# Optimization experiments

Hardware: AMD Instinct MI355X
Metric: run time of the kernel (lower is better)

Reference implementation:

```python
import jax, jax.numpy as jnp
import numpy as np
from jax import lax

T, B, H, L = 512, 64, 512, 2  # seq_len, batch, hidden(=input), num_layers


def setup_inputs() -> dict:
    key = jax.random.key(0)
    ks = jax.random.split(key, 6)
    s = 1.0 / np.sqrt(H)  # torch default init scale
    x = jax.random.normal(ks[0], (T, B, H), dtype=jnp.float32)
    h0 = jax.random.normal(ks[1], (L, B, H), dtype=jnp.float32)
    W_ih = jax.random.uniform(ks[2], (L, H, H), jnp.float32, -s, s)
    W_hh = jax.random.uniform(ks[3], (L, H, H), jnp.float32, -s, s)
    b_ih = jax.random.uniform(ks[4], (L, H), jnp.float32, -s, s)
    b_hh = jax.random.uniform(ks[5], (L, H), jnp.float32, -s, s)
    return {"x": x, "h0": h0, "W_ih": W_ih, "W_hh": W_hh, "b_ih": b_ih, "b_hh": b_hh}


def _run_layer(x, h0, Wi, Wh, bi, bh):
    # Precompute input contribution for all timesteps: [T,B,H]
    xw = jnp.einsum('tbi,hi->tbh', x, Wi) + bi

    def step(h, xw_t):
        h_new = jnp.tanh(xw_t + h @ Wh.T + bh)
        return h_new, h_new

    h_last, ys = lax.scan(step, h0, xw)
    return ys, h_last


def reference(x, h0, W_ih, W_hh, b_ih, b_hh):
    # Multi-layer Elman RNN with tanh, matching torch.nn.RNN (batch_first=False).
    h_n = []
    out = x
    for l in range(L):
        out, h_last = _run_layer(out, h0[l], W_ih[l], W_hh[l], b_ih[l], b_hh[l])
        h_n.append(h_last)
    return out, jnp.stack(h_n, axis=0)
```

## Files before the change

### kernel.cpp

```cpp
#include <hip/hip_runtime.h>
#include <stdint.h>

#define T_ 512
#define B_ 64
#define H_ 512
#define L_ 2
#define TBH (T_*B_*H_)
#define BH  (B_*H_)
#define NC  8
#define CS  64
#define CROWS (CS*B_)
#define CSZ ((size_t)CROWS*H_)
#define WPK_OFF  ((size_t)4*CSZ)
#define WPK_U4L  (64*512)
#define WIHP_OFF (WPK_OFF + (size_t)2*WPK_U4L*4)
#define Y1_OFF   (WIHP_OFF + (size_t)262144)
#define Y1SZ     ((size_t)CROWS*H_)

typedef float    f32x4 __attribute__((ext_vector_type(4)));
typedef short    s16x8 __attribute__((ext_vector_type(8)));
typedef short    s16x4 __attribute__((ext_vector_type(4)));
typedef _Float16 h2    __attribute__((ext_vector_type(2)));

static __device__ __forceinline__ short f2bf(float f) {
  uint32_t u = __float_as_uint(f);
  u = (u + 0x7fffu + ((u >> 16) & 1u)) >> 16;
  return (short)u;
}

static __device__ __forceinline__ float fdot2(h2 a, h2 b, float c) {
#if __has_builtin(__builtin_amdgcn_fdot2)
  return __builtin_amdgcn_fdot2(a, b, c, false);
#else
  return c + (float)a[0] * (float)b[0] + (float)a[1] * (float)b[1];
#endif
}

template <int IMM>
static __device__ __forceinline__ float swz(float v) {
  return __int_as_float(__builtin_amdgcn_ds_swizzle(__float_as_int(v), IMM));
}

static __device__ __forceinline__ float dpp_xor1(float v) {
  return __int_as_float(__builtin_amdgcn_mov_dpp(__float_as_int(v), 0xB1, 0xF, 0xF, true));
}
static __device__ __forceinline__ float dpp_xor2(float v) {
  return __int_as_float(__builtin_amdgcn_mov_dpp(__float_as_int(v), 0x4E, 0xF, 0xF, true));
}

static __device__ __forceinline__ void rawbar() {
  __builtin_amdgcn_sched_barrier(0);
  asm volatile("s_waitcnt lgkmcnt(0)" ::: "memory");
  __builtin_amdgcn_s_barrier();
  __builtin_amdgcn_sched_barrier(0);
}

static __device__ __forceinline__ uint32_t pack2(float a, float b) {
  h2 p = { (_Float16)a, (_Float16)b };
  return __builtin_bit_cast(uint32_t, p);
}

static __device__ __forceinline__ h2 bch(uint32_t u) {
  return __builtin_bit_cast(h2, u);
}

__global__ __launch_bounds__(512, 1)
void prepack(const float* __restrict__ Whh, const float* __restrict__ Wih,
             const float* __restrict__ x, float* __restrict__ ws,
             float* __restrict__ out) {
  const int bid = blockIdx.x, tid = threadIdx.x;
  if (bid < 2) {
    const int l = bid, c = tid & 7, rg = tid >> 3;
    uint4* dst = (uint4*)(ws + WPK_OFF) + (size_t)l * WPK_U4L;
    const float* W = Whh + (size_t)l * H_ * H_;
    #pragma unroll
    for (int k = 0; k < 8; ++k) {
      const float* wrow = W + (size_t)(rg * 8 + k) * H_ + c * 64;
      #pragma unroll
      for (int u = 0; u < 6; ++u) {
        f32x4 w4 = *(const f32x4*)(wrow + u * 8);
        f32x4 w5 = *(const f32x4*)(wrow + u * 8 + 4);
        uint4 pk;
        pk.x = pack2(w4.x, w4.y);
        pk.y = pack2(w4.z, w4.w);
        pk.z = pack2(w5.x, w5.y);
        pk.w = pack2(w5.z, w5.w);
        dst[(k * 6 + u) * 512 + tid] = pk;
      }
      #pragma unroll
      for (int p = 0; p < 2; ++p) {
        f32x4 w4 = *(const f32x4*)(wrow + 48 + p * 8);
        f32x4 w5 = *(const f32x4*)(wrow + 48 + p * 8 + 4);
        uint4 pk;
        pk.x = pack2(w4.x, w4.y);
        pk.y = pack2(w4.z, w4.w);
        pk.z = pack2(w5.x, w5.y);
        pk.w = pack2(w5.z, w5.w);
        dst[(48 + k * 2 + p) * 512 + tid] = pk;
      }
    }
  } else if (bid < 4) {
    const int l = bid - 2;
    const float* src = Wih + (size_t)l * H_ * H_;
    short* dst = (short*)(ws + WIHP_OFF) + (size_t)l * H_ * H_;
    for (int it = 0; it < 64; ++it) {
      int e = (it * 512 + tid) * 8;
      f32x4 a = *(const f32x4*)(src + e);
      f32x4 b = *(const f32x4*)(src + e + 4);
      s16x8 p = { f2bf(a.x), f2bf(a.y), f2bf(a.z), f2bf(a.w),
                  f2bf(b.x), f2bf(b.y), f2bf(b.z), f2bf(b.w) };
      *(s16x8*)(dst + e) = p;
    }
  } else {
    const int w = bid - 4;
    const int cc = w >> 3, sub = w & 7;
    const float* src = x + (size_t)cc * CSZ + (size_t)sub * (CSZ / 8);
    short* dst = (short*)(out + (size_t)cc * CSZ) + (size_t)sub * (CSZ / 8);
    for (int it = 0; it < 64; ++it) {
      int e = (it * 512 + tid) * 8;
      f32x4 a = *(const f32x4*)(src + e);
      f32x4 b = *(const f32x4*)(src + e + 4);
      s16x8 p = { f2bf(a.x), f2bf(a.y), f2bf(a.z), f2bf(a.w),
                  f2bf(b.x), f2bf(b.y), f2bf(b.z), f2bf(b.w) };
      *(s16x8*)(dst + e) = p;
    }
  }
}

__device__ void gemm_role(char* smem, int rb,
                          const short* __restrict__ In,
                          const short* __restrict__ W,
                          const float* __restrict__ bi,
                          const float* __restrict__ bh,
                          float* __restrict__ Out) {
  constexpr int LDT = 40;
  short* As = (short*)smem;
  short* Bs = (short*)(smem + 256 * LDT * 2);

  const int tid  = threadIdx.x;
  const int m0   = (rb >> 2) * 256;
  const int n0   = (rb & 3) * 128;
  const int wave = tid >> 6, lane = tid & 63;
  const int wm   = (wave >> 1) * 64;
  const int wn   = (wave & 1) * 64;
  const int quad = lane >> 4, tq = lane & 15;

  f32x4 acc[4][4] = {};

  for (int k0 = 0; k0 < 512; k0 += 32) {
    #pragma unroll
    for (int v = 0; v < 2; ++v) {
      int idx = v * 512 + tid;
      int r = idx >> 2, cc = (idx & 3) * 8;
      s16x8 a = *(const s16x8*)(In + (size_t)(m0 + r) * 512 + k0 + cc);
      *(s16x8*)(&As[r * LDT + cc]) = a;
    }
    {
      int r = tid >> 2, cc = (tid & 3) * 8;
      s16x8 b = *(const s16x8*)(W + (size_t)(n0 + r) * 512 + k0 + cc);
      *(s16x8*)(&Bs[r * LDT + cc]) = b;
    }
    __syncthreads();

    s16x8 af[4], bfr[4];
    #pragma unroll
    for (int mf = 0; mf < 4; ++mf)
      af[mf] = *(const s16x8*)(&As[(wm + mf * 16 + tq) * LDT + quad * 8]);
    #pragma unroll
    for (int nf = 0; nf < 4; ++nf)
      bfr[nf] = *(const s16x8*)(&Bs[(wn + nf * 16 + tq) * LDT + quad * 8]);
    #pragma unroll
    for (int mf = 0; mf < 4; ++mf)
      #pragma unroll
      for (int nf = 0; nf < 4; ++nf)
        acc[mf][nf] = __builtin_amdgcn_mfma_f32_16x16x32_bf16(
            af[mf], bfr[nf], acc[mf][nf], 0, 0, 0);
    __syncthreads();
  }

  #pragma unroll
  for (int nf = 0; nf < 4; ++nf) {
    int col = n0 + wn + nf * 16 + tq;
    float bv = bi[col] + bh[col];
    #pragma unroll
    for (int mf = 0; mf < 4; ++mf) {
      #pragma unroll
      for (int r = 0; r < 4; ++r) {
        int row = m0 + wm + mf * 16 + quad * 4 + r;
        Out[(size_t)row * 512 + col] = acc[mf][nf][r] + bv;
      }
    }
  }
}

template <bool BF16Y>
__device__ void recur_role(char* smem, int b, int chunk,
                           float* __restrict__ xw_y,
                           short* __restrict__ yb,
                           const float* __restrict__ h0l,
                           const uint4* __restrict__ wpk,
                           float* __restrict__ hstate) {
  const int tid = threadIdx.x;
  const int c   = tid & 7;

  uint4*    wlds = (uint4*)smem;
  _Float16* hbuf = (_Float16*)(smem + 131072);

  const uint4* wp = wpk + tid;
  h2 wreg[8][24];
  #pragma unroll
  for (int k = 0; k < 8; ++k)
    #pragma unroll
    for (int u = 0; u < 6; ++u) {
      uint4 v = wp[(k * 6 + u) * 512];
      wreg[k][u * 4 + 0] = bch(v.x);
      wreg[k][u * 4 + 1] = bch(v.y);
      wreg[k][u * 4 + 2] = bch(v.z);
      wreg[k][u * 4 + 3] = bch(v.w);
    }
  #pragma unroll
  for (int j = 0; j < 16; ++j)
    wlds[j * 512 + tid] = wp[(48 + j) * 512];

  float hini = (chunk == 0) ? h0l[b * 512 + tid] : hstate[b * 512 + tid];
  hbuf[(tid >> 6) * 72 + (tid & 63)] = (_Float16)hini;
  __syncthreads();

#define UBLK(HV, W0)                                                        \
  { h2 p0 = bch((HV).x), p1 = bch((HV).y), p2 = bch((HV).z), p3 = bch((HV).w); \
    _Pragma("unroll")                                                       \
    for (int k = 0; k < 8; ++k) {                                           \
      acc[k] = fdot2(wreg[k][(W0) + 0], p0, acc[k]);                        \
      acc[k] = fdot2(wreg[k][(W0) + 1], p1, acc[k]);                        \
      acc[k] = fdot2(wreg[k][(W0) + 2], p2, acc[k]);                        \
      acc[k] = fdot2(wreg[k][(W0) + 3], p3, acc[k]);                        \
    } }

#define WLDX(g)                                                             \
  { wt0 = wlds[(4 * (g) + 0) * 512 + tid];                                  \
    wt1 = wlds[(4 * (g) + 1) * 512 + tid];                                  \
    wt2 = wlds[(4 * (g) + 2) * 512 + tid];                                  \
    wt3 = wlds[(4 * (g) + 3) * 512 + tid]; }

#define CONSX(K0)                                                           \
  { h2 q0 = bch(q4.x), q1 = bch(q4.y), q2 = bch(q4.z), q3 = bch(q4.w);      \
    h2 r0 = bch(r4.x), r1 = bch(r4.y), r2 = bch(r4.z), r3 = bch(r4.w);      \
    float a = acc[(K0)];                                                    \
    a = fdot2(bch(wt0.x), q0, a); a = fdot2(bch(wt0.y), q1, a);             \
    a = fdot2(bch(wt0.z), q2, a); a = fdot2(bch(wt0.w), q3, a);             \
    a = fdot2(bch(wt1.x), r0, a); a = fdot2(bch(wt1.y), r1, a);             \
    a = fdot2(bch(wt1.z), r2, a); a = fdot2(bch(wt1.w), r3, a);             \
    acc[(K0)] = a;                                                          \
    a = acc[(K0) + 1];                                                      \
    a = fdot2(bch(wt2.x), q0, a); a = fdot2(bch(wt2.y), q1, a);             \
    a = fdot2(bch(wt2.z), q2, a); a = fdot2(bch(wt2.w), q3, a);             \
    a = fdot2(bch(wt3.x), r0, a); a = fdot2(bch(wt3.y), r1, a);             \
    a = fdot2(bch(wt3.z), r2, a); a = fdot2(bch(wt3.w), r3, a);             \
    acc[(K0) + 1] = a; }

  const float* xwp = xw_y + (size_t)b * 512 + tid;
  float xwv = xwp[0];
  float hlast = 0.f;
  for (int ls = 0; ls < CS; ++ls) {
    const int cur = ls & 1, nxt = cur ^ 1;
    int tn = (ls + 1 < CS) ? ls + 1 : ls;
    float xwn = xwp[(size_t)tn * BH];

    const _Float16* hc = &hbuf[cur * 8 * 72 + c * 72];
#define HLD(i) (*(const uint4*)(hc + (i) * 8))

    float acc[8] = {0, 0, 0, 0, 0, 0, 0, 0};

    uint4 ha = HLD(0), hbv = HLD(1), hx = HLD(2);
    uint4 q4 = HLD(6), r4 = HLD(7);
    uint4 wt0, wt1, wt2, wt3;

    WLDX(0);
    UBLK(ha, 0);   ha  = HLD(3);
    CONSX(0);      WLDX(1);
    UBLK(hbv, 4);  hbv = HLD(4);
    CONSX(2);      WLDX(2);
    UBLK(hx, 8);   hx  = HLD(5);
    CONSX(4);      WLDX(3);
    UBLK(ha, 12);
    CONSX(6);
    UBLK(hbv, 16);
    UBLK(hx, 20);

    float r1v[4];
    #pragma unroll
    for (int p = 0; p < 4; ++p) {
      float send = (c & 1) ? acc[2 * p] : acc[2 * p + 1];
      float recv = dpp_xor1(send);
      float keep = (c & 1) ? acc[2 * p + 1] : acc[2 * p];
      r1v[p] = keep + recv;
    }
    float r2v[2];
    #pragma unroll
    for (int p = 0; p < 2; ++p) {
      float send = (c & 2) ? r1v[2 * p] : r1v[2 * p + 1];
      float recv = dpp_xor2(send);
      float keep = (c & 2) ? r1v[2 * p + 1] : r1v[2 * p];
      r2v[p] = keep + recv;
    }
    {
      float send = (c & 4) ? r2v[0] : r2v[1];
      float recv = swz<0x101F>(send);
      float keep = (c & 4) ? r2v[1] : r2v[0];
      float dot  = keep + recv;

      float pre = dot + xwv;
      float e   = __expf(2.f * pre);
      float hni = 1.f - 2.f / (e + 1.f);
      hbuf[nxt * 8 * 72 + (tid >> 6) * 72 + (tid & 63)] = (_Float16)hni;
      if constexpr (BF16Y)
        yb[(size_t)ls * BH + b * 512 + tid] = f2bf(hni);
      else
        xw_y[(size_t)ls * BH + b * 512 + tid] = hni;
      hlast = hni;
    }
    rawbar();
    xwv = xwn;
#undef HLD
  }
  hstate[b * 512 + tid] = hlast;
#undef UBLK
#undef WLDX
#undef CONSX
}

__global__ __launch_bounds__(512, 1)
void stage(int s, const float* __restrict__ h0,
           const float* __restrict__ bih, const float* __restrict__ bhh,
           float* __restrict__ ws, float* __restrict__ out) {
  __shared__ __align__(16) char smem[133376];
  const int role = blockIdx.x >> 6;
  const int rb   = blockIdx.x & 63;
  float* hn = out + (size_t)TBH;
  const uint4* wpk  = (const uint4*)(ws + WPK_OFF);
  const short* wihp = (const short*)(ws + WIHP_OFF);
  short*       y1b  = (short*)(ws + Y1_OFF);

  if (role == 0) {
    int cc = s;
    if (cc < 0 || cc >= NC) return;
    recur_role<true>(smem, rb, cc, ws + (size_t)(cc & 3) * CSZ,
                     y1b + (size_t)(cc & 3) * Y1SZ, h0, wpk, hn);
  } else if (role == 1) {
    int cc = s - 2;
    if (cc < 0 || cc >= NC) return;
    recur_role<false>(smem, rb, cc, out + (size_t)cc * CSZ, nullptr,
                      h0 + BH, wpk + WPK_U4L, hn + BH);
  } else if (role == 2) {
    int cc = s + 1;
    if (cc < 0 || cc >= NC) return;
    gemm_role(smem, rb, (const short*)(out + (size_t)cc * CSZ), wihp,
              bih, bhh, ws + (size_t)(cc & 3) * CSZ);
  } else {
    int cc = s - 1;
    if (cc < 0 || cc >= NC) return;
    gemm_role(smem, rb, y1b + (size_t)(cc & 3) * Y1SZ,
              wihp + (size_t)H_ * H_, bih + H_, bhh + H_,
              out + (size_t)cc * CSZ);
  }
}

extern "C" void kernel_launch(void* const* d_in, const int* in_sizes, int n_in,
                              void* d_out, int out_size, void* d_ws, size_t ws_size,
                              hipStream_t stream) {
  const float* x   = (const float*)d_in[0];
  const float* h0  = (const float*)d_in[1];
  const float* Wih = (const float*)d_in[2];
  const float* Whh = (const float*)d_in[3];
  const float* bih = (const float*)d_in[4];
  const float* bhh = (const float*)d_in[5];
  float* out = (float*)d_out;
  float* ws  = (float*)d_ws;

  prepack<<<68, 512, 0, stream>>>(Whh, Wih, x, ws, out);
  for (int s = -1; s <= NC + 1; ++s)
    stage<<<256, 512, 0, stream>>>(s, h0, bih, bhh, ws, out);
}
```

Before: 1.119 ms.

## Overlap layer-1 input GEMM with layer-0 recurrence via in-kernel progress flags

Layer-0 recurrence blocks publish a per-16-timestep progress counter with release atomics. Layer-1 GEMM blocks for the same chunk spin on those counters, so they can run in the same stage launch instead of one stage later. The pipeline therefore loses one stage and one kernel launch. In exchange it relies on all 256 blocks being co-resident so the spin-waits cannot deadlock, and it adds a memset plus extra barriers and fences every 16 steps.

```diff
diff --git a/kernel.cpp b/kernel.cpp
--- a/kernel.cpp
+++ b/kernel.cpp
@@ -16,6 +16,7 @@
 #define WIHP_OFF (WPK_OFF + (size_t)2*WPK_U4L*4)
 #define Y1_OFF   (WIHP_OFF + (size_t)262144)
 #define Y1SZ     ((size_t)CROWS*H_)
+#define FLG_OFF  (Y1_OFF + (size_t)2*Y1SZ)
 
 typedef float    f32x4 __attribute__((ext_vector_type(4)));
 typedef short    s16x8 __attribute__((ext_vector_type(8)));
@@ -53,6 +54,16 @@
   asm volatile("s_waitcnt lgkmcnt(0)" ::: "memory");
   __builtin_amdgcn_s_barrier();
   __builtin_amdgcn_sched_barrier(0);
+}
+
+static __device__ __forceinline__ void waitg(uint32_t* c, uint32_t tgt) {
+  if (threadIdx.x == 0) {
+    while (__hip_atomic_load(c, __ATOMIC_RELAXED, __HIP_MEMORY_SCOPE_AGENT) < tgt)
+      __builtin_amdgcn_s_sleep(16);
+    (void)__hip_atomic_load(c, __ATOMIC_ACQUIRE, __HIP_MEMORY_SCOPE_AGENT);
+  }
+  __syncthreads();
+  __threadfence();
 }
 
 static __device__ __forceinline__ uint32_t pack2(float a, float b) {
@@ -197,6 +208,7 @@
 __device__ void recur_role(char* smem, int b, int chunk,
                            float* __restrict__ xw_y,
                            short* __restrict__ yb,
+                           uint32_t* __restrict__ yflag,
                            const float* __restrict__ h0l,
                            const uint4* __restrict__ wpk,
                            float* __restrict__ hstate) {
@@ -319,7 +331,15 @@
         xw_y[(size_t)ls * BH + b * 512 + tid] = hni;
       hlast = hni;
     }
-    rawbar();
+    if (BF16Y && ((ls & 15) == 15)) {
+      __syncthreads();
+      __threadfence();
+      if (tid == 0)
+        __hip_atomic_fetch_add(&yflag[ls >> 4], 1u,
+                               __ATOMIC_RELEASE, __HIP_MEMORY_SCOPE_AGENT);
+    } else {
+      rawbar();
+    }
     xwv = xwn;
 #undef HLD
   }
@@ -340,16 +360,18 @@
   const uint4* wpk  = (const uint4*)(ws + WPK_OFF);
   const short* wihp = (const short*)(ws + WIHP_OFF);
   short*       y1b  = (short*)(ws + Y1_OFF);
+  uint32_t*    yfl  = (uint32_t*)(ws + FLG_OFF);
 
   if (role == 0) {
     int cc = s;
     if (cc < 0 || cc >= NC) return;
     recur_role<true>(smem, rb, cc, ws + (size_t)(cc & 3) * CSZ,
-                     y1b + (size_t)(cc & 3) * Y1SZ, h0, wpk, hn);
+                     y1b + (size_t)(cc & 3) * Y1SZ, yfl + cc * 4,
+                     h0, wpk, hn);
   } else if (role == 1) {
-    int cc = s - 2;
+    int cc = s - 1;
     if (cc < 0 || cc >= NC) return;
-    recur_role<false>(smem, rb, cc, out + (size_t)cc * CSZ, nullptr,
+    recur_role<false>(smem, rb, cc, out + (size_t)cc * CSZ, nullptr, nullptr,
                       h0 + BH, wpk + WPK_U4L, hn + BH);
   } else if (role == 2) {
     int cc = s + 1;
@@ -357,8 +379,11 @@
     gemm_role(smem, rb, (const short*)(out + (size_t)cc * CSZ), wihp,
               bih, bhh, ws + (size_t)(cc & 3) * CSZ);
   } else {
-    int cc = s - 1;
+    int cc = s;
     if (cc < 0 || cc >= NC) return;
+    int tile = rb >> 2;
+    int q = (4 * tile + 3) >> 4;
+    waitg(&yfl[cc * 4 + q], 64u);
     gemm_role(smem, rb, y1b + (size_t)(cc & 3) * Y1SZ,
               wihp + (size_t)H_ * H_, bih + H_, bhh + H_,
               out + (size_t)cc * CSZ);
@@ -377,7 +402,8 @@
   float* out = (float*)d_out;
   float* ws  = (float*)d_ws;
 
+  hipMemsetAsync((char*)d_ws + FLG_OFF * sizeof(float), 0, 256, stream);
   prepack<<<68, 512, 0, stream>>>(Whh, Wih, x, ws, out);
-  for (int s = -1; s <= NC + 1; ++s)
+  for (int s = -1; s <= NC; ++s)
     stage<<<256, 512, 0, stream>>>(s, h0, bih, bhh, ws, out);
 }
```

Measured after the change: 1.625 ms. 45.3% more time.
